# Optimization experiments

Hardware: AMD Instinct MI355X
Metric: run time of the kernel (lower is better)

Reference implementation:

```python
import jax, jax.numpy as jnp
import numpy as np

FS = 64      # FIGURE_SEZE
HALF = 32    # FS // 2
STD = 12     # STD_LEN
BATCH = 4    # BATCH_SIZE
EPS = 1e-3   # keras BatchNormalization default epsilon
CC = 256     # cycleCount (multiple of BATCH)
D = FS * HALF  # 2048, dense in/out width


def _split(x):
    # Checkerboard boolean-mask gather: mask[i,j] = ((i + j) % 2 == 0).
    # Row-major flatten of data[mask] -> for even rows take even cols, odd rows odd cols.
    x4 = x.reshape(-1, FS, HALF, 2)                    # [N, FS, HALF, 2]
    par = (jnp.arange(FS) % 2)[None, :, None, None]    # per-row column parity
    u1 = jnp.take_along_axis(x4, par, axis=3)[..., 0]  # masked half   [N, FS, HALF]
    u2 = jnp.take_along_axis(x4, 1 - par, axis=3)[..., 0]  # demasked half
    return u1, u2


def _bn_dense(u, p):
    # computeF/computeG: flatten -> inference BatchNorm -> Dense(2048) -> reshape
    g, be, m, v, W, b = p
    s = u.reshape(u.shape[0], D)
    s = g * (s - m) * jax.lax.rsqrt(v + EPS) + be
    s = s @ W + b
    return s.reshape(-1, FS, HALF)


def _spread(w, off):
    # w @ expandM: place the 32 columns of w at columns off, off+2, ... of a 64-wide zero mat
    z = jnp.zeros((w.shape[0], FS, FS), w.dtype)
    return z.at[:, :, off::2].set(w)


def _move_even(mat, d):
    # keep even rows; roll odd rows along the column axis by d (== tf diag-matmul + roll)
    even = (jnp.arange(FS) % 2 == 0)[:, None]
    return jnp.where(even, mat, jnp.roll(mat, d, axis=2))


def _mix(w1, w2):
    return _move_even(_spread(w1, 0), -1) + _move_even(_spread(w2, 1), 1)


def _encoder(x, F, G):
    u1, u2 = _split(x.reshape(-1, FS, FS))
    v1 = u1 + _bn_dense(u2, F)
    w2 = u2 + _bn_dense(v1, G)
    return _mix(v1, w2).reshape(-1, STD, FS, FS)


def _decoder(y, F, G):
    w1, w2 = _split(y.reshape(-1, FS, FS))
    v2 = w2 - _bn_dense(w1, G)
    u1 = w1 - _bn_dense(v2, F)
    return _mix(u1, v2).reshape(-1, STD, FS, FS)


def _forward(inputs, W1, b1, g1, be1, m1, v1, W3, b3, g3, be3, m3, v3, kop):
    x = inputs                                   # [CC, STD, FS, FS]
    cc = x.shape[0]
    F = (g1, be1, m1, v1, W1, b1)
    G = (g3, be3, m3, v3, W3, b3)
    phiX = _encoder(x, F, G)
    dephiPhiX = _decoder(phiX, F, G)
    # Koopman step: reshape to [BATCH, cc//BATCH, ...], transpose, right-multiply K
    p = phiX.reshape(BATCH, cc // BATCH, STD, FS, FS).transpose(1, 0, 2, 3, 4)
    kPhix = (p @ kop).reshape(-1, STD, FS, FS)
    dePhiKPhiX = _decoder(kPhix, F, G)
    return (x, phiX, dephiPhiX, kPhix, dePhiKPhiX, x[:, 1:], phiX[:, 1:])


def setup_inputs() -> dict:
    key = jax.random.key(0)
    ks = jax.random.split(key, 16)
    inp = {
        "inputs": jax.random.normal(ks[0], (CC, STD, FS, FS), jnp.float32),
        "indexs": jax.random.randint(ks[1], (CC,), 0, 100),  # unused by forward
        "W1": jax.random.normal(ks[2], (D, 2048), jnp.float32) * 0.02,
        "b1": jnp.zeros((2048,), jnp.float32),
        "g1": jax.random.uniform(ks[3], (D,), jnp.float32, 0.9, 1.1),
        "be1": jax.random.normal(ks[4], (D,), jnp.float32) * 0.01,
        "m1": jax.random.normal(ks[5], (D,), jnp.float32) * 0.01,
        "v1": jax.random.uniform(ks[6], (D,), jnp.float32, 0.5, 1.5),
        "W3": jax.random.normal(ks[7], (D, 2048), jnp.float32) * 0.02,
        "b3": jnp.zeros((2048,), jnp.float32),
        "g3": jax.random.uniform(ks[8], (D,), jnp.float32, 0.9, 1.1),
        "be3": jax.random.normal(ks[9], (D,), jnp.float32) * 0.01,
        "m3": jax.random.normal(ks[10], (D,), jnp.float32) * 0.01,
        "v3": jax.random.uniform(ks[11], (D,), jnp.float32, 0.5, 1.5),
        "kop": jax.random.normal(ks[12], (FS, FS), jnp.float32) * 0.125,
    }
    return inp


def reference(inputs, indexs, W1, b1, g1, be1, m1, v1, W3, b3, g3, be3, m3, v3, kop):
    del indexs  # unused in the original call()
    return _forward(inputs, W1, b1, g1, be1, m1, v1, W3, b3, g3, be3, m3, v3, kop)
```

## Files before the change

kernel.cpp:

```cpp
#include <hip/hip_runtime.h>

#define DDIM 2048
#define NROWS 3072

typedef float f32x4 __attribute__((ext_vector_type(4)));
typedef __bf16 bf16x8 __attribute__((ext_vector_type(8)));

__device__ __forceinline__ unsigned short f32_bf16(float f) {
    unsigned int u = __float_as_uint(f);
    u += 0x7fffu + ((u >> 16) & 1u);
    return (unsigned short)(u >> 16);
}

__device__ __forceinline__ void gl2lds16(const unsigned short* g, unsigned short* l) {
    __builtin_amdgcn_global_load_lds(
        (__attribute__((address_space(1))) void*)g,
        (__attribute__((address_space(3))) void*)l, 16, 0, 0);
}

__global__ __launch_bounds__(256) void prep_scal(
    const float* __restrict__ g1, const float* __restrict__ be1,
    const float* __restrict__ m1, const float* __restrict__ v1,
    const float* __restrict__ b1, float* __restrict__ a1, float* __restrict__ c1, float* __restrict__ bp1,
    const float* __restrict__ g3, const float* __restrict__ be3,
    const float* __restrict__ m3, const float* __restrict__ v3,
    const float* __restrict__ b3, float* __restrict__ a3, float* __restrict__ c3, float* __restrict__ bp3)
{
    int n = blockIdx.x * 256 + threadIdx.x;
    if (n < DDIM) {
        float av1 = g1[n] / sqrtf(v1[n] + 1e-3f);
        a1[n] = av1; c1[n] = be1[n] - m1[n] * av1; bp1[n] = b1[n];
        float av3 = g3[n] / sqrtf(v3[n] + 1e-3f);
        a3[n] = av3; c3[n] = be3[n] - m3[n] * av3; bp3[n] = b3[n];
    }
}

__global__ __launch_bounds__(256) void prep_w(
    const float* __restrict__ W, const float* __restrict__ a, const float* __restrict__ c,
    unsigned short* __restrict__ Wt, float* __restrict__ bp)
{
    __shared__ float tile[64][65];
    __shared__ float red[4][64];
    const int kt = blockIdx.x * 64, nt = blockIdx.y * 64;
    const int t = threadIdx.x;
    float part = 0.f;
#pragma unroll
    for (int q = 0; q < 16; ++q) {
        int lin = q * 256 + t;
        int r = lin >> 6, cl = lin & 63;
        float w = W[(size_t)(kt + r) * DDIM + nt + cl];
        tile[r][cl] = a[kt + r] * w;
        part += c[kt + r] * w;
    }
    red[t >> 6][t & 63] = part;
    __syncthreads();
    if (t < 64) {
        float s = red[0][t] + red[1][t] + red[2][t] + red[3][t];
        atomicAdd(&bp[nt + t], s);
    }
#pragma unroll
    for (int q = 0; q < 16; ++q) {
        int lin = q * 256 + t;
        int r = lin >> 6, cl = lin & 63;
        Wt[(size_t)(nt + r) * DDIM + kt + cl] = f32_bf16(tile[cl][r]);
    }
}

__global__ __launch_bounds__(256) void split_x(
    const float* __restrict__ x, float* __restrict__ o0,
    float* __restrict__ o5, unsigned short* __restrict__ u2b)
{
    int idx = blockIdx.x * 256 + threadIdx.x;
    int n = idx >> 10, rem = idx & 1023, i = rem >> 4, h2 = rem & 15;
    int base = (n << 12) + (i << 6) + (h2 << 2);
    f32x4 xv = *(const f32x4*)(x + base);
    *(f32x4*)(o0 + base) = xv;
    int cc = n / 12, s = n - cc * 12;
    if (s >= 1) {
        int tb = ((cc * 11 + (s - 1)) << 12) + (i << 6) + (h2 << 2);
        *(f32x4*)(o5 + tb) = xv;
    }
    unsigned int w0, w1;
    if ((i & 1) == 0) { w0 = f32_bf16(xv[1]); w1 = f32_bf16(xv[3]); }
    else             { w0 = f32_bf16(xv[0]); w1 = f32_bf16(xv[2]); }
    *(unsigned int*)(u2b + (size_t)n * DDIM + (i << 5) + (h2 << 1)) = w0 | (w1 << 16);
}

__global__ __launch_bounds__(256) void koop_k(
    const float* __restrict__ phiX, const float* __restrict__ kop,
    float* __restrict__ out, unsigned short* __restrict__ Wb)
{
    __shared__ float P[64][65];
    __shared__ alignas(16) float Kp[64][64];
    const int t = threadIdx.x;
    const int np = blockIdx.x;
    int ccp = np / 12, s = np - ccp * 12;
    int src = (((ccp & 3) << 6) + (ccp >> 2)) * 12 + s;
    const float* Ps = phiX + (size_t)src * 4096;
#pragma unroll
    for (int q = 0; q < 16; ++q) {
        int lin = q * 256 + t, r = lin >> 6, c = lin & 63;
        P[r][c] = Ps[lin];
        Kp[r][c] = kop[lin];
    }
    __syncthreads();
    const int jq = (t & 15) << 2;
    const int i0 = (t >> 4) << 2;
    f32x4 acc[4];
#pragma unroll
    for (int r = 0; r < 4; ++r) acc[r] = f32x4{0.f, 0.f, 0.f, 0.f};
    for (int k = 0; k < 64; ++k) {
        f32x4 kv = *(const f32x4*)&Kp[k][jq];
#pragma unroll
        for (int r = 0; r < 4; ++r) acc[r] += P[i0 + r][k] * kv;
    }
    float* o = out + (size_t)np * 4096;
#pragma unroll
    for (int r = 0; r < 4; ++r) {
        const int i = i0 + r;
        *(f32x4*)(o + i * 64 + jq) = acc[r];
        const int par = i & 1;
        unsigned int w0 = f32_bf16(acc[r][par]);
        unsigned int w1v = f32_bf16(acc[r][2 + par]);
        *(unsigned int*)(Wb + (size_t)np * 2048 + i * 32 + (jq >> 1)) = w0 | (w1v << 16);
    }
}

template<int MODE>
__global__ __launch_bounds__(256, 3) void gemm_k(
    const unsigned short* __restrict__ Abf, const unsigned short* __restrict__ Wt,
    const float* __restrict__ bp, const float* __restrict__ resid0, const float* __restrict__ resid1,
    float* __restrict__ out0, float* __restrict__ out1,
    unsigned short* __restrict__ cb0, unsigned short* __restrict__ cb1,
    const float* __restrict__ partner)
{
    constexpr int PARX = (MODE == 1 || MODE == 2) ? 1 : 0;
    constexpr bool NEG  = (MODE >= 2);
    constexpr bool DUAL = (MODE >= 2);

    __shared__ alignas(16) unsigned short As[128][64];
    __shared__ alignas(16) unsigned short Bs[128][64];
    const int t = threadIdx.x;
    const int lane = t & 63, wave = t >> 6;
    const int quad = lane >> 4, l16 = lane & 15;
    const int m0 = blockIdx.x * 128;
    const int n0 = blockIdx.y * 128;
    const int wm = (wave >> 1) << 6;
    const int wn = (wave & 1) << 6;

    const int srow = lane >> 3;
    const int cdata = (lane & 7) ^ srow;
    const unsigned short* Ag = Abf + (size_t)(m0 + wave * 32 + srow) * DDIM + (cdata << 3);
    const unsigned short* Bg = Wt  + (size_t)(n0 + wave * 32 + srow) * DDIM + (cdata << 3);
    unsigned short* AslBase = &As[wave * 32][0];
    unsigned short* BslBase = &Bs[wave * 32][0];

    f32x4 acc[4][4];
#pragma unroll
    for (int a = 0; a < 4; ++a)
#pragma unroll
        for (int b = 0; b < 4; ++b) acc[a][b] = f32x4{0.f, 0.f, 0.f, 0.f};

    for (int k0 = 0; k0 < DDIM; k0 += 64) {
        __syncthreads();
#pragma unroll
        for (int j = 0; j < 4; ++j) {
            gl2lds16(Ag + (size_t)(j * 8) * DDIM + k0, AslBase + j * 8 * 64);
            gl2lds16(Bg + (size_t)(j * 8) * DDIM + k0, BslBase + j * 8 * 64);
        }
        __syncthreads();

#pragma unroll
        for (int kk = 0; kk < 2; ++kk) {
            bf16x8 af[4], bfr[4];
#pragma unroll
            for (int mi = 0; mi < 4; ++mi) {
                const int r = wm + mi * 16 + l16;
                af[mi] = *(const bf16x8*)&As[r][(((kk << 2) | quad) ^ (l16 & 7)) << 3];
            }
#pragma unroll
            for (int ni = 0; ni < 4; ++ni) {
                const int r = wn + ni * 16 + l16;
                bfr[ni] = *(const bf16x8*)&Bs[r][(((kk << 2) | quad) ^ (l16 & 7)) << 3];
            }
#pragma unroll
            for (int mi = 0; mi < 4; ++mi)
#pragma unroll
                for (int ni = 0; ni < 4; ++ni)
                    acc[mi][ni] = __builtin_amdgcn_mfma_f32_16x16x32_bf16(
                        af[mi], bfr[ni], acc[mi][ni], 0, 0, 0);
        }
    }

    const bool second = DUAL && (m0 >= NROWS);

#pragma unroll
    for (int ni = 0; ni < 4; ++ni) {
        const int n = n0 + wn + ni * 16 + l16;
        const float bias = bp[n];
        const int i = n >> 5, h = n & 31;
        const int par = (i & 1) ^ PARX;
#pragma unroll
        for (int mi = 0; mi < 4; ++mi) {
            const int mbase = m0 + wm + mi * 16 + (quad << 2);
#pragma unroll
            for (int r = 0; r < 4; ++r) {
                const int mm = mbase + r;
                const int mloc = second ? (mm - NROWS) : mm;
                float cv = acc[mi][ni][r] + bias;
                const float* rrow = (DUAL ? (second ? resid1 : resid0) : resid0)
                                    + ((size_t)(DUAL ? mloc : mm) << 12);
                float rs = rrow[(i << 6) + (h << 1) + par];
                float o = NEG ? (rs - cv) : (rs + cv);
                if constexpr (MODE == 0) {
                    out0[(size_t)mm * DDIM + n] = o;
                    unsigned short us = f32_bf16(o);
                    cb0[(size_t)mm * DDIM + n] = us;
                    const int hw = (h - (i & 1)) & 31;
                    cb1[(size_t)mm * DDIM + (i << 5) + hw] = us;
                } else if constexpr (MODE == 2) {
                    out0[(size_t)mm * DDIM + n] = o;
                    cb0[(size_t)mm * DDIM + n] = f32_bf16(o);
                } else if constexpr (MODE == 1) {
                    float2 f2; int col;
                    if ((i & 1) == 0) {
                        col = h << 1;
                        f2.x = partner[(size_t)mm * DDIM + n];
                        f2.y = o;
                    } else {
                        col = ((h + 1) & 31) << 1;
                        f2.x = o;
                        f2.y = partner[(size_t)mm * DDIM + (i << 5) + ((h + 2) & 31)];
                    }
                    *(float2*)(out0 + ((size_t)mm << 12) + (i << 6) + col) = f2;
                    int cc = mm / 12, s = mm - cc * 12;
                    if (s >= 1)
                        *(float2*)(out1 + ((size_t)(cc * 11 + s - 1) << 12) + (i << 6) + col) = f2;
                } else {
                    float2 f2; int col;
                    if ((i & 1) == 0) {
                        col = h << 1;
                        f2.x = o;
                        f2.y = partner[(size_t)mm * DDIM + n];
                    } else {
                        col = ((h + 31) & 31) << 1;
                        f2.x = partner[(size_t)mm * DDIM + (i << 5) + ((h + 30) & 31)];
                        f2.y = o;
                    }
                    float* yb = second ? out1 : out0;
                    *(float2*)(yb + ((size_t)mloc << 12) + (i << 6) + col) = f2;
                }
            }
        }
    }
}

extern "C" void kernel_launch(void* const* d_in, const int* in_sizes, int n_in,
                              void* d_out, int out_size, void* d_ws, size_t ws_size,
                              hipStream_t stream)
{
    (void)in_sizes; (void)n_in; (void)out_size; (void)ws_size;
    const float* x   = (const float*)d_in[0];
    const float* W1  = (const float*)d_in[2];
    const float* b1  = (const float*)d_in[3];
    const float* g1  = (const float*)d_in[4];
    const float* be1 = (const float*)d_in[5];
    const float* m1  = (const float*)d_in[6];
    const float* v1i = (const float*)d_in[7];
    const float* W3  = (const float*)d_in[8];
    const float* b3  = (const float*)d_in[9];
    const float* g3  = (const float*)d_in[10];
    const float* be3 = (const float*)d_in[11];
    const float* m3  = (const float*)d_in[12];
    const float* v3i = (const float*)d_in[13];
    const float* kop = (const float*)d_in[14];

    float* out = (float*)d_out;
    float* o0 = out;
    float* o1 = out + 12582912;
    float* o2 = out + 25165824;
    float* o3 = out + 37748736;
    float* o4 = out + 50331648;
    float* o5 = out + 62914560;
    float* o6 = out + 74448896;

    char* ws = (char*)d_ws;
    float* a1  = (float*)(ws);
    float* c1  = (float*)(ws + 8192);
    float* a3  = (float*)(ws + 16384);
    float* c3  = (float*)(ws + 24576);
    float* bp1 = (float*)(ws + 32768);
    float* bp3 = (float*)(ws + 40960);
    unsigned short* Wt1 = (unsigned short*)(ws + 49152);
    unsigned short* Wt3 = (unsigned short*)(ws + 8437760);
    unsigned short* Abf = (unsigned short*)(ws + 16826368);
    unsigned short* Mbf = (unsigned short*)(ws + 29409280);
    unsigned short* Dbf = (unsigned short*)(ws + 41992192);
    unsigned short* Kbf = (unsigned short*)(ws + 54575104);
    float* Fa  = (float*)(ws + 67158016);
    float* Ga  = (float*)(ws + 67158016);
    unsigned short* Gbf = (unsigned short*)(ws + 16826368);

    prep_scal<<<8, 256, 0, stream>>>(g1, be1, m1, v1i, b1, a1, c1, bp1,
                                     g3, be3, m3, v3i, b3, a3, c3, bp3);
    prep_w<<<dim3(32, 32), 256, 0, stream>>>(W1, a1, c1, Wt1, bp1);
    prep_w<<<dim3(32, 32), 256, 0, stream>>>(W3, a3, c3, Wt3, bp3);
    split_x<<<12288, 256, 0, stream>>>(x, o0, o5, Abf);

    const dim3 ge(24, 16);
    const dim3 gd(48, 16);

    gemm_k<0><<<ge, 256, 0, stream>>>(Abf, Wt1, bp1, x, nullptr, Fa, nullptr, Mbf, Dbf, nullptr);
    gemm_k<1><<<ge, 256, 0, stream>>>(Mbf, Wt3, bp3, x, nullptr, o1, o6, nullptr, nullptr, Fa);

    koop_k<<<3072, 256, 0, stream>>>(o1, kop, o3, Kbf);

    gemm_k<2><<<gd, 256, 0, stream>>>(Dbf, Wt3, bp3, o1, o3, Ga, nullptr, Gbf, nullptr, nullptr);
    gemm_k<3><<<gd, 256, 0, stream>>>(Gbf, Wt1, bp1, o1, o3, o2, o4, nullptr, nullptr, Ga);
}
```

Before: 874.2 us.

## Add 256x256 pipelined GEMM for decoder, swizzle block order, merge prep_w launches

Adds a new 512-thread GEMM kernel with 256x256 tiles, 128KB of dynamic LDS, double buffering via direct global-to-LDS loads, explicit barrier-staged phases and MFMA priority hints. The two decoder GEMMs (6144 rows) now use it, which raises data reuse per tile and overlaps loads with compute. The encoder GEMMs switch to a 1D grid with a swizzled block order aimed at better L2 locality, and the two weight-prep launches are merged into one grid using the z dimension. The larger kernel cuts occupancy and its hand-written waitcnt and barrier scheduling is fragile.

```diff
diff --git a/kernel.cpp b/kernel.cpp
--- a/kernel.cpp
+++ b/kernel.cpp
@@ -36,9 +36,17 @@
 }
 
 __global__ __launch_bounds__(256) void prep_w(
-    const float* __restrict__ W, const float* __restrict__ a, const float* __restrict__ c,
-    unsigned short* __restrict__ Wt, float* __restrict__ bp)
-{
+    const float* __restrict__ W1, const float* __restrict__ a1, const float* __restrict__ c1,
+    unsigned short* __restrict__ Wt1, float* __restrict__ bp1,
+    const float* __restrict__ W3, const float* __restrict__ a3, const float* __restrict__ c3,
+    unsigned short* __restrict__ Wt3, float* __restrict__ bp3)
+{
+    const float* W = blockIdx.z ? W3 : W1;
+    const float* a = blockIdx.z ? a3 : a1;
+    const float* c = blockIdx.z ? c3 : c1;
+    unsigned short* Wt = blockIdx.z ? Wt3 : Wt1;
+    float* bp = blockIdx.z ? bp3 : bp1;
+
     __shared__ float tile[64][65];
     __shared__ float red[4][64];
     const int kt = blockIdx.x * 64, nt = blockIdx.y * 64;
@@ -129,22 +137,22 @@
 template<int MODE>
 __global__ __launch_bounds__(256, 3) void gemm_k(
     const unsigned short* __restrict__ Abf, const unsigned short* __restrict__ Wt,
-    const float* __restrict__ bp, const float* __restrict__ resid0, const float* __restrict__ resid1,
+    const float* __restrict__ bp, const float* __restrict__ resid0,
     float* __restrict__ out0, float* __restrict__ out1,
     unsigned short* __restrict__ cb0, unsigned short* __restrict__ cb1,
     const float* __restrict__ partner)
 {
-    constexpr int PARX = (MODE == 1 || MODE == 2) ? 1 : 0;
-    constexpr bool NEG  = (MODE >= 2);
-    constexpr bool DUAL = (MODE >= 2);
+    constexpr int PARX = (MODE == 1) ? 1 : 0;
 
     __shared__ alignas(16) unsigned short As[128][64];
     __shared__ alignas(16) unsigned short Bs[128][64];
     const int t = threadIdx.x;
     const int lane = t & 63, wave = t >> 6;
     const int quad = lane >> 4, l16 = lane & 15;
-    const int m0 = blockIdx.x * 128;
-    const int n0 = blockIdx.y * 128;
+    const int id = blockIdx.x;
+    const int swz = (id & 7) * 48 + (id >> 3);
+    const int m0 = (swz % 24) << 7;
+    const int n0 = (swz / 24) << 7;
     const int wm = (wave >> 1) << 6;
     const int wn = (wave & 1) << 6;
 
@@ -192,8 +200,6 @@
         }
     }
 
-    const bool second = DUAL && (m0 >= NROWS);
-
 #pragma unroll
     for (int ni = 0; ni < 4; ++ni) {
         const int n = n0 + wn + ni * 16 + l16;
@@ -206,22 +212,16 @@
 #pragma unroll
             for (int r = 0; r < 4; ++r) {
                 const int mm = mbase + r;
-                const int mloc = second ? (mm - NROWS) : mm;
                 float cv = acc[mi][ni][r] + bias;
-                const float* rrow = (DUAL ? (second ? resid1 : resid0) : resid0)
-                                    + ((size_t)(DUAL ? mloc : mm) << 12);
-                float rs = rrow[(i << 6) + (h << 1) + par];
-                float o = NEG ? (rs - cv) : (rs + cv);
+                float rs = resid0[((size_t)mm << 12) + (i << 6) + (h << 1) + par];
+                float o = rs + cv;
                 if constexpr (MODE == 0) {
                     out0[(size_t)mm * DDIM + n] = o;
                     unsigned short us = f32_bf16(o);
                     cb0[(size_t)mm * DDIM + n] = us;
                     const int hw = (h - (i & 1)) & 31;
                     cb1[(size_t)mm * DDIM + (i << 5) + hw] = us;
-                } else if constexpr (MODE == 2) {
-                    out0[(size_t)mm * DDIM + n] = o;
-                    cb0[(size_t)mm * DDIM + n] = f32_bf16(o);
-                } else if constexpr (MODE == 1) {
+                } else {
                     float2 f2; int col;
                     if ((i & 1) == 0) {
                         col = h << 1;
@@ -235,7 +235,124 @@
                     *(float2*)(out0 + ((size_t)mm << 12) + (i << 6) + col) = f2;
                     int cc = mm / 12, s = mm - cc * 12;
                     if (s >= 1)
-                        *(float2*)(out1 + ((size_t)(cc * 11 + s - 1) << 12) + (i << 6) + col) = f2;
+                        *(float2*)(out1 + (((size_t)(cc * 11 + s - 1) << 12) + (i << 6) + col)) = f2;
+                }
+            }
+        }
+    }
+}
+
+template<int MODE>
+__global__ __launch_bounds__(512, 2) void gemm256_k(
+    const unsigned short* __restrict__ Abf, const unsigned short* __restrict__ Wt,
+    const float* __restrict__ bp, const float* __restrict__ resid0, const float* __restrict__ resid1,
+    float* __restrict__ out0, float* __restrict__ out1,
+    unsigned short* __restrict__ cb0, const float* __restrict__ partner)
+{
+    constexpr int PARX = (MODE == 2) ? 1 : 0;
+    extern __shared__ unsigned short S[];
+
+    const int t = threadIdx.x;
+    const int lane = t & 63, wave = t >> 6;
+    const int quad = lane >> 4, l16 = lane & 15;
+    const int wm = wave >> 2, wn = wave & 3;
+    const int id = blockIdx.x;
+    const int swz = (id & 7) * 24 + (id >> 3);
+    const int m0 = (swz % 24) << 8;
+    const int n0 = (swz / 24) << 8;
+
+    const int srow = lane >> 2, schunk = lane & 3;
+    const unsigned short* Ag = Abf + (size_t)(m0 + wave * 32 + srow) * DDIM + schunk * 8;
+    const unsigned short* Bg = Wt  + (size_t)(n0 + wave * 32 + srow) * DDIM + schunk * 8;
+
+    f32x4 acc[8][4];
+#pragma unroll
+    for (int a = 0; a < 8; ++a)
+#pragma unroll
+        for (int b = 0; b < 4; ++b) acc[a][b] = f32x4{0.f, 0.f, 0.f, 0.f};
+
+    auto stage = [&](int buf, int slot, const unsigned short* g, int koff) __attribute__((always_inline)) {
+        unsigned short* d = &S[(((buf << 2) | slot) << 13) + wave * 1024];
+        gl2lds16(g + koff, d);
+        gl2lds16(g + koff + 16 * DDIM, d + 512);
+    };
+    auto phase_mfma = [&](int buf, int kk, int H) __attribute__((always_inline)) {
+        bf16x8 a_[4], b_[4];
+        const int sa = (((buf << 2) | (kk << 1)) << 13) + (wm * 128 + H * 64 + l16) * 32 + quad * 8;
+        const int sb = ((((buf << 2) | (kk << 1)) | 1) << 13) + (wn * 64 + l16) * 32 + quad * 8;
+#pragma unroll
+        for (int mi = 0; mi < 4; ++mi) a_[mi] = *(const bf16x8*)&S[sa + mi * 512];
+#pragma unroll
+        for (int ni = 0; ni < 4; ++ni) b_[ni] = *(const bf16x8*)&S[sb + ni * 512];
+        __builtin_amdgcn_s_setprio(1);
+#pragma unroll
+        for (int mi = 0; mi < 4; ++mi)
+#pragma unroll
+            for (int ni = 0; ni < 4; ++ni)
+                acc[H * 4 + mi][ni] = __builtin_amdgcn_mfma_f32_16x16x32_bf16(
+                    a_[mi], b_[ni], acc[H * 4 + mi][ni], 0, 0, 0);
+        __builtin_amdgcn_s_setprio(0);
+    };
+
+    stage(0, 0, Ag, 0);
+    stage(0, 1, Bg, 0);
+    stage(0, 2, Ag, 32);
+    stage(0, 3, Bg, 32);
+
+    for (int T = 0; T < 31; ++T) {
+        const int buf = T & 1, nb = buf ^ 1;
+        const int kt = (T + 1) * 64;
+        asm volatile("s_waitcnt vmcnt(4)" ::: "memory");
+        __builtin_amdgcn_s_barrier();
+        __builtin_amdgcn_sched_barrier(0);
+        stage(nb, 0, Ag, kt);
+        phase_mfma(buf, 0, 0);
+        __builtin_amdgcn_s_barrier();
+        __builtin_amdgcn_sched_barrier(0);
+        stage(nb, 1, Bg, kt);
+        phase_mfma(buf, 0, 1);
+        asm volatile("s_waitcnt vmcnt(4)" ::: "memory");
+        __builtin_amdgcn_s_barrier();
+        __builtin_amdgcn_sched_barrier(0);
+        stage(nb, 2, Ag, kt + 32);
+        phase_mfma(buf, 1, 0);
+        __builtin_amdgcn_s_barrier();
+        __builtin_amdgcn_sched_barrier(0);
+        stage(nb, 3, Bg, kt + 32);
+        phase_mfma(buf, 1, 1);
+    }
+    asm volatile("s_waitcnt vmcnt(4)" ::: "memory");
+    __builtin_amdgcn_s_barrier(); __builtin_amdgcn_sched_barrier(0);
+    phase_mfma(1, 0, 0);
+    __builtin_amdgcn_s_barrier(); __builtin_amdgcn_sched_barrier(0);
+    phase_mfma(1, 0, 1);
+    asm volatile("s_waitcnt vmcnt(0)" ::: "memory");
+    __builtin_amdgcn_s_barrier(); __builtin_amdgcn_sched_barrier(0);
+    phase_mfma(1, 1, 0);
+    __builtin_amdgcn_s_barrier(); __builtin_amdgcn_sched_barrier(0);
+    phase_mfma(1, 1, 1);
+
+    const bool second = (m0 >= NROWS);
+#pragma unroll
+    for (int ni = 0; ni < 4; ++ni) {
+        const int n = n0 + wn * 64 + ni * 16 + l16;
+        const float bias = bp[n];
+        const int i = n >> 5, h = n & 31;
+        const int par = (i & 1) ^ PARX;
+#pragma unroll
+        for (int a = 0; a < 8; ++a) {
+            const int mbase = m0 + wm * 128 + (a >> 2) * 64 + (a & 3) * 16 + (quad << 2);
+#pragma unroll
+            for (int r = 0; r < 4; ++r) {
+                const int mm = mbase + r;
+                const int mloc = second ? (mm - NROWS) : mm;
+                float cv = acc[a][ni][r] + bias;
+                const float* rrow = (second ? resid1 : resid0) + ((size_t)mloc << 12);
+                float rs = rrow[(i << 6) + (h << 1) + par];
+                float o = rs - cv;
+                if constexpr (MODE == 2) {
+                    out0[(size_t)mm * DDIM + n] = o;
+                    cb0[(size_t)mm * DDIM + n] = f32_bf16(o);
                 } else {
                     float2 f2; int col;
                     if ((i & 1) == 0) {
@@ -301,20 +418,26 @@
     float* Ga  = (float*)(ws + 67158016);
     unsigned short* Gbf = (unsigned short*)(ws + 16826368);
 
+    static bool attr_set = false;
+    if (!attr_set) {
+        hipFuncSetAttribute(reinterpret_cast<const void*>(gemm256_k<2>),
+                            hipFuncAttributeMaxDynamicSharedMemorySize, 131072);
+        hipFuncSetAttribute(reinterpret_cast<const void*>(gemm256_k<3>),
+                            hipFuncAttributeMaxDynamicSharedMemorySize, 131072);
+        attr_set = true;
+    }
+
     prep_scal<<<8, 256, 0, stream>>>(g1, be1, m1, v1i, b1, a1, c1, bp1,
                                      g3, be3, m3, v3i, b3, a3, c3, bp3);
-    prep_w<<<dim3(32, 32), 256, 0, stream>>>(W1, a1, c1, Wt1, bp1);
-    prep_w<<<dim3(32, 32), 256, 0, stream>>>(W3, a3, c3, Wt3, bp3);
+    prep_w<<<dim3(32, 32, 2), 256, 0, stream>>>(W1, a1, c1, Wt1, bp1,
+                                                W3, a3, c3, Wt3, bp3);
     split_x<<<12288, 256, 0, stream>>>(x, o0, o5, Abf);
 
-    const dim3 ge(24, 16);
-    const dim3 gd(48, 16);
-
-    gemm_k<0><<<ge, 256, 0, stream>>>(Abf, Wt1, bp1, x, nullptr, Fa, nullptr, Mbf, Dbf, nullptr);
-    gemm_k<1><<<ge, 256, 0, stream>>>(Mbf, Wt3, bp3, x, nullptr, o1, o6, nullptr, nullptr, Fa);
+    gemm_k<0><<<384, 256, 0, stream>>>(Abf, Wt1, bp1, x, Fa, nullptr, Mbf, Dbf, nullptr);
+    gemm_k<1><<<384, 256, 0, stream>>>(Mbf, Wt3, bp3, x, o1, o6, nullptr, nullptr, Fa);
 
     koop_k<<<3072, 256, 0, stream>>>(o1, kop, o3, Kbf);
 
-    gemm_k<2><<<gd, 256, 0, stream>>>(Dbf, Wt3, bp3, o1, o3, Ga, nullptr, Gbf, nullptr, nullptr);
-    gemm_k<3><<<gd, 256, 0, stream>>>(Gbf, Wt1, bp1, o1, o3, o2, o4, nullptr, nullptr, Ga);
-}
+    gemm256_k<2><<<192, 512, 131072, stream>>>(Dbf, Wt3, bp3, o1, o3, Ga, nullptr, Gbf, nullptr);
+    gemm256_k<3><<<192, 512, 131072, stream>>>(Gbf, Wt1, bp1, o1, o3, o2, o4, nullptr, Ga);
+}
```

Result: slower. 952.7 us (+9.0%).
